# Kernel optimization log

Hardware: AMD Instinct MI355X
Metric: run time of the kernel (lower is better)

Reference implementation:

```python
import jax, jax.numpy as jnp
import numpy as np

N, E = 50000, 800000
DN, DE, H = 128, 64, 96


def _glorot(key, shape):
    fan_in = shape[0] if len(shape) > 1 else shape[0]
    return jax.random.normal(key, shape, jnp.float32) * (1.0 / np.sqrt(fan_in))


def setup_inputs() -> dict:
    key = jax.random.key(0)
    ks = jax.random.split(key, 24)
    inp = {
        "x": jax.random.normal(ks[0], (N, DN), jnp.float32),
        "edge_index": jax.random.randint(ks[1], (2, E), 0, N, jnp.int32),
        "edge_attr": jax.random.normal(ks[2], (E, DE), jnp.float32),
        # GATConv layer 0 (heads=1): lin [DN,H], lin_edge [DE,H], att vectors [H], bias [H]
        "w0": _glorot(ks[3], (DN, H)),
        "we0": _glorot(ks[4], (DE, H)),
        "as0": _glorot(ks[5], (H,)),
        "ad0": _glorot(ks[6], (H,)),
        "ae0": _glorot(ks[7], (H,)),
        "b0": jnp.zeros((H,), jnp.float32),
        # edge update 0: Linear(2H+DE -> H)
        "ew0": _glorot(ks[8], (2 * H + DE, H)),
        "eb0": jnp.zeros((H,), jnp.float32),
        # GATConv layer 1: lin [H,H], lin_edge [H,H]
        "w1": _glorot(ks[9], (H, H)),
        "we1": _glorot(ks[10], (H, H)),
        "as1": _glorot(ks[11], (H,)),
        "ad1": _glorot(ks[12], (H,)),
        "ae1": _glorot(ks[13], (H,)),
        "b1": jnp.zeros((H,), jnp.float32),
        # edge update 1: Linear(3H -> H)
        "ew1": _glorot(ks[14], (3 * H, H)),
        "eb1": jnp.zeros((H,), jnp.float32),
    }
    return inp


def gat_conv(x, src, dst, ea, W, We, a_s, a_d, a_e, b, n):
    """PyG GATConv, heads=1, eval mode, add_self_loops with fill_value='mean'."""
    ne = ea.shape[0]
    # self-loop edge attr = mean of incoming edge features per destination node
    cnt = jax.ops.segment_sum(jnp.ones((ne,), ea.dtype), dst, num_segments=n)
    loop_ea = jax.ops.segment_sum(ea, dst, num_segments=n) / jnp.maximum(cnt, 1.0)[:, None]
    ar = jnp.arange(n, dtype=src.dtype)
    sa = jnp.concatenate([src, ar])            # [E+N] augmented source idx
    da = jnp.concatenate([dst, ar])            # [E+N] augmented dest idx
    eaa = jnp.concatenate([ea, loop_ea], axis=0)
    h = x @ W                                   # [N,H]
    ep = eaa @ We                               # [E+N,H]
    logits = jax.nn.leaky_relu((h @ a_s)[sa] + (h @ a_d)[da] + ep @ a_e, 0.2)
    m = jax.ops.segment_max(logits, da, num_segments=n)
    p = jnp.exp(logits - m[da])
    denom = jax.ops.segment_sum(p, da, num_segments=n)
    alpha = p / denom[da]                       # segment softmax over dst neighborhoods
    return jax.ops.segment_sum(alpha[:, None] * h[sa], da, num_segments=n) + b


def reference(x, edge_index, edge_attr,
              w0, we0, as0, ad0, ae0, b0, ew0, eb0,
              w1, we1, as1, ad1, ae1, b1, ew1, eb1):
    src, dst = edge_index[0], edge_index[1]
    n = x.shape[0]
    # layer 0
    x = gat_conv(x, src, dst, edge_attr, w0, we0, as0, ad0, ae0, b0, n)
    edge_attr = jnp.concatenate([x[src], x[dst], edge_attr], axis=1) @ ew0 + eb0
    # layer 1
    x = gat_conv(x, src, dst, edge_attr, w1, we1, as1, ad1, ae1, b1, n)
    edge_attr = jnp.concatenate([x[src], x[dst], edge_attr], axis=1) @ ew1 + eb1
    return (x, edge_attr)
```

## Files before the change

kernel.cpp:

```cpp
#include <hip/hip_runtime.h>
#include <math.h>

#define NN 50000
#define NE 800000
#define DNODE 128
#define DEDGE 64
#define HD 96

__device__ __forceinline__ float lrelu(float x){ return x > 0.f ? x : 0.2f*x; }

__global__ void k_count(const int* __restrict__ dst, int* __restrict__ cnt){
  int e = blockIdx.x*256 + threadIdx.x;
  if (e < NE) atomicAdd(&cnt[dst[e]], 1);
}

__global__ __launch_bounds__(1024) void k_scan(const int* __restrict__ cnt,
                                               int* __restrict__ rowptr){
  __shared__ int wsum[16];
  __shared__ int carry_s;
  const int t = threadIdx.x;
  const int lane = t & 63, w = t >> 6;
  if (t == 0) carry_s = 0;
  __syncthreads();
  const int nch = (NN + 1023)/1024;
  for (int c=0;c<nch;c++){
    int i = c*1024 + t;
    int v = (i < NN) ? cnt[i] : 0;
    int s = v;
    #pragma unroll
    for (int o=1;o<64;o<<=1){
      int u = __shfl_up(s, o, 64);
      if (lane >= o) s += u;
    }
    if (lane == 63) wsum[w] = s;
    __syncthreads();
    if (t < 16){
      int x = wsum[t];
      #pragma unroll
      for (int o=1;o<16;o<<=1){
        int u = __shfl_up(x, o, 64);
        if (t >= o) x += u;
      }
      wsum[t] = x;
    }
    __syncthreads();
    int total = wsum[15];
    int base = carry_s + (w ? wsum[w-1] : 0);
    if (i < NN) rowptr[i] = base + s - v;
    __syncthreads();
    if (t == 0) carry_s += total;
  }
  __syncthreads();
  if (t == 0) rowptr[NN] = carry_s;
}

__global__ void k_fill(const int* __restrict__ src, const int* __restrict__ dst,
                       const int* __restrict__ rowptr, int* __restrict__ fillc,
                       int* __restrict__ perm, int* __restrict__ src_s){
  int e = blockIdx.x*256 + threadIdx.x;
  if (e >= NE) return;
  int d = dst[e];
  int pos = rowptr[d] + atomicAdd(&fillc[d], 1);
  perm[pos]  = e;
  src_s[pos] = src[e];
}

__global__ void k_vec(const float* __restrict__ We, const float* __restrict__ ae,
                      float* __restrict__ v, int K){
  int k = threadIdx.x;
  if (k < K){
    float s = 0.f;
    for (int j=0;j<HD;j++) s += We[k*HD + j]*ae[j];
    v[k] = s;
  }
}

__global__ void k_elr(const float* __restrict__ Ein, const float* __restrict__ v,
                      float* __restrict__ elr, int K){
  int e = blockIdx.x*256 + threadIdx.x;
  if (e >= NE) return;
  const float4* row = (const float4*)(Ein + (size_t)e*K);
  float s = 0.f;
  for (int k=0;k<K/4;k++){
    float4 a = row[k];
    float4 b = ((const float4*)v)[k];
    s += a.x*b.x + a.y*b.y + a.z*b.z + a.w*b.w;
  }
  elr[e] = s;
}

template<int K, bool DOTS>
__global__ __launch_bounds__(256,4) void k_nodegemm_t(const float* __restrict__ X,
    const float* __restrict__ W, float* __restrict__ Y, int M,
    const float* __restrict__ va, const float* __restrict__ vb,
    float* __restrict__ hs, float* __restrict__ hd){
  __shared__ float Wl[K*HD];
  for (int idx=threadIdx.x; idx<K*HD/4; idx+=256)
    ((float4*)Wl)[idx] = ((const float4*)W)[idx];
  __syncthreads();
  const int r  = threadIdx.x >> 3;
  const int c0 = (threadIdx.x & 7)*12;
  const int r0 = blockIdx.x*128 + r;
  float acc[4][12];
  #pragma unroll
  for (int q=0;q<4;q++)
    #pragma unroll
    for (int j=0;j<12;j++) acc[q][j]=0.f;
  for (int k=0;k<K;k+=4){
    float4 xv[4];
    #pragma unroll
    for (int q=0;q<4;q++){
      int row = r0 + 32*q;
      xv[q] = (row < M) ? *(const float4*)(X + (size_t)row*K + k)
                        : make_float4(0.f,0.f,0.f,0.f);
    }
    #pragma unroll
    for (int kk=0;kk<4;kk++){
      float wv[12];
      const float* wr = Wl + (k+kk)*HD + c0;
      #pragma unroll
      for (int j=0;j<12;j++) wv[j] = wr[j];
      #pragma unroll
      for (int q=0;q<4;q++){
        float xs = ((const float*)&xv[q])[kk];
        #pragma unroll
        for (int j=0;j<12;j++) acc[q][j] += xs*wv[j];
      }
    }
  }
  float vva[12], vvb[12];
  if constexpr (DOTS){
    #pragma unroll
    for (int j=0;j<12;j++){ vva[j]=va[c0+j]; vvb[j]=vb[c0+j]; }
  }
  #pragma unroll
  for (int q=0;q<4;q++){
    int row = r0 + 32*q;
    if (row >= M) continue;
    float* yr = Y + (size_t)row*HD + c0;
    float d1=0.f, d2=0.f;
    #pragma unroll
    for (int j=0;j<12;j++){
      float o = acc[q][j];
      yr[j] = o;
      if constexpr (DOTS){ d1 += o*vva[j]; d2 += o*vvb[j]; }
    }
    if constexpr (DOTS){
      #pragma unroll
      for (int o=1;o<8;o<<=1){ d1 += __shfl_xor(d1,o,64); d2 += __shfl_xor(d2,o,64); }
      if ((threadIdx.x&7)==0){ hs[row]=d1; hd[row]=d2; }
    }
  }
}

template<int K, bool ELR>
__global__ __launch_bounds__(256,4) void k_edgegemm_t(const float* __restrict__ Ein,
    const float* __restrict__ W,
    const float* __restrict__ A, const float* __restrict__ B,
    const int* __restrict__ src, const int* __restrict__ dst,
    const float* __restrict__ bias, float* __restrict__ Out,
    const float* __restrict__ v, float* __restrict__ elr){
  __shared__ float Wl[K*HD];
  for (int idx=threadIdx.x; idx<K*HD/4; idx+=256)
    ((float4*)Wl)[idx] = ((const float4*)W)[idx];
  __syncthreads();
  const int r  = threadIdx.x >> 3;
  const int c0 = (threadIdx.x & 7)*12;
  const int e0 = blockIdx.x*128 + r;
  float acc[4][12];
  #pragma unroll
  for (int q=0;q<4;q++)
    #pragma unroll
    for (int j=0;j<12;j++) acc[q][j]=0.f;
  const float* e_base = Ein + (size_t)e0*K;
  for (int k=0;k<K;k+=4){
    float4 xv[4];
    #pragma unroll
    for (int q=0;q<4;q++)
      xv[q] = *(const float4*)(e_base + (size_t)(32*q)*K + k);
    #pragma unroll
    for (int kk=0;kk<4;kk++){
      float wv[12];
      const float* wr = Wl + (k+kk)*HD + c0;
      #pragma unroll
      for (int j=0;j<12;j++) wv[j] = wr[j];
      #pragma unroll
      for (int q=0;q<4;q++){
        float xs = ((const float*)&xv[q])[kk];
        #pragma unroll
        for (int j=0;j<12;j++) acc[q][j] += xs*wv[j];
      }
    }
  }
  __syncthreads();
  float bj[12], vv[12];
  #pragma unroll
  for (int j=0;j<12;j++) bj[j] = bias[c0+j];
  if constexpr (ELR){
    #pragma unroll
    for (int j=0;j<12;j++) vv[j] = v[c0+j];
  }
  #pragma unroll
  for (int q=0;q<4;q++){
    int e = e0 + 32*q;
    int s = src[e], d = dst[e];
    const float* Ar = A + (size_t)s*HD + c0;
    const float* Br = B + (size_t)d*HD + c0;
    float* orow = Out + (size_t)e*HD + c0;
    float pd = 0.f;
    #pragma unroll
    for (int j=0;j<12;j++){
      float o = acc[q][j] + Ar[j] + Br[j] + bj[j];
      orow[j] = o;
      if constexpr (ELR) pd += o*vv[j];
    }
    if constexpr (ELR){
      pd += __shfl_xor(pd,1,64);
      pd += __shfl_xor(pd,2,64);
      pd += __shfl_xor(pd,4,64);
      if ((threadIdx.x&7)==0) elr[e] = pd;
    }
  }
}

__global__ __launch_bounds__(256) void k_gat(const int* __restrict__ rowptr,
    const int* __restrict__ src_s, const int* __restrict__ perm,
    const float* __restrict__ hs, const float* __restrict__ hd,
    const float* __restrict__ elr,
    const float* __restrict__ h, const float* __restrict__ bias,
    float* __restrict__ Out){
  int lane = threadIdx.x & 63;
  int n = blockIdx.x*4 + (threadIdx.x >> 6);
  if (n >= NN) return;
  int beg = rowptr[n], end = rowptr[n+1];
  float hdn = hd[n];
  float mxn = -INFINITY;
  float se  = 0.f;
  for (int i = beg + lane; i < end; i += 64){
    float el = elr[perm[i]];
    se += el;
    mxn = fmaxf(mxn, lrelu(hs[src_s[i]] + hdn + el));
  }
  #pragma unroll
  for (int o=32;o>0;o>>=1){
    mxn = fmaxf(mxn, __shfl_xor(mxn, o, 64));
    se += __shfl_xor(se, o, 64);
  }
  float slp = se / fmaxf((float)(end-beg), 1.f);
  float selfL = lrelu(hs[n] + hdn + slp);
  float mx = fmaxf(mxn, selfL);
  float acc0 = 0.f, acc1 = 0.f, denom = 0.f;
  for (int i = beg; i < end; ++i){
    int s = src_s[i];
    float p = __expf(lrelu(hs[s] + hdn + elr[perm[i]]) - mx);
    denom += p;
    acc0 += p * h[(size_t)s*HD + lane];
    if (lane < 32) acc1 += p * h[(size_t)s*HD + 64 + lane];
  }
  float ps = __expf(selfL - mx);
  denom += ps;
  acc0 += ps * h[(size_t)n*HD + lane];
  if (lane < 32) acc1 += ps * h[(size_t)n*HD + 64 + lane];
  float inv = 1.f/denom;
  Out[(size_t)n*HD + lane] = acc0*inv + bias[lane];
  if (lane < 32) Out[(size_t)n*HD + 64 + lane] = acc1*inv + bias[64+lane];
}

extern "C" void kernel_launch(void* const* d_in, const int* in_sizes, int n_in,
                              void* d_out, int out_size, void* d_ws, size_t ws_size,
                              hipStream_t stream){
  const float* x   = (const float*)d_in[0];
  const int*   ei  = (const int*)d_in[1];
  const float* ea  = (const float*)d_in[2];
  const float* w0  = (const float*)d_in[3];
  const float* we0 = (const float*)d_in[4];
  const float* as0 = (const float*)d_in[5];
  const float* ad0 = (const float*)d_in[6];
  const float* ae0 = (const float*)d_in[7];
  const float* b0  = (const float*)d_in[8];
  const float* ew0 = (const float*)d_in[9];
  const float* eb0 = (const float*)d_in[10];
  const float* w1  = (const float*)d_in[11];
  const float* we1 = (const float*)d_in[12];
  const float* as1 = (const float*)d_in[13];
  const float* ad1 = (const float*)d_in[14];
  const float* ae1 = (const float*)d_in[15];
  const float* b1  = (const float*)d_in[16];
  const float* ew1 = (const float*)d_in[17];
  const float* eb1 = (const float*)d_in[18];

  const int* srcp = ei;
  const int* dstp = ei + NE;

  char* ws = (char*)d_ws;
  size_t off = 0;
  auto carve = [&](size_t bytes)->char*{
    char* p = ws + off; off += (bytes + 255) & ~(size_t)255; return p;
  };
  int*   rowptr = (int*)carve(4ull*(NN+1));
  int*   fillc  = (int*)carve(4ull*NN);
  int*   perm   = (int*)carve(4ull*NE);
  int*   src_s  = (int*)carve(4ull*NE);
  float* hbuf   = (float*)carve(4ull*NN*HD);
  float* x0     = (float*)carve(4ull*NN*HD);
  float* Ab     = (float*)carve(4ull*NN*HD);
  float* Bb     = (float*)carve(4ull*NN*HD);
  float* hsb    = (float*)carve(4ull*NN);
  float* hdb    = (float*)carve(4ull*NN);
  float* elr    = (float*)carve(4ull*NE);
  float* vsm0   = (float*)carve(4ull*128);
  float* vsm1   = (float*)carve(4ull*128);
  (void)ws_size; (void)in_sizes; (void)n_in; (void)out_size;

  float* xout  = (float*)d_out;
  float* eaout = (float*)d_out + (size_t)NN*HD;

  const int EB  = (NE + 255)/256;
  const int GE  = NE/128;
  const int GN  = (NN + 127)/128;

  hipMemsetAsync(fillc, 0, 4ull*NN, stream);
  k_count<<<EB, 256, 0, stream>>>(dstp, fillc);
  k_scan<<<1, 1024, 0, stream>>>(fillc, rowptr);
  hipMemsetAsync(fillc, 0, 4ull*NN, stream);
  k_fill<<<EB, 256, 0, stream>>>(srcp, dstp, rowptr, fillc, perm, src_s);

  k_vec<<<1, 128, 0, stream>>>(we0, ae0, vsm0, DEDGE);
  k_vec<<<1, 128, 0, stream>>>(we1, ae1, vsm1, HD);

  k_elr<<<EB, 256, 0, stream>>>(ea, vsm0, elr, DEDGE);
  k_nodegemm_t<DNODE,true><<<GN, 256, 0, stream>>>(x, w0, hbuf, NN, as0, ad0, hsb, hdb);
  k_gat<<<(NN+3)/4, 256, 0, stream>>>(rowptr, src_s, perm, hsb, hdb, elr, hbuf, b0, x0);

  k_nodegemm_t<HD,false><<<GN, 256, 0, stream>>>(x0, ew0,         Ab, NN, nullptr, nullptr, nullptr, nullptr);
  k_nodegemm_t<HD,false><<<GN, 256, 0, stream>>>(x0, ew0 + 96*HD, Bb, NN, nullptr, nullptr, nullptr, nullptr);
  k_edgegemm_t<DEDGE,true><<<GE, 256, 0, stream>>>(ea, ew0 + 192*HD, Ab, Bb, srcp, dstp,
                                                   eb0, eaout, vsm1, elr);

  k_nodegemm_t<HD,true><<<GN, 256, 0, stream>>>(x0, w1, hbuf, NN, as1, ad1, hsb, hdb);
  k_gat<<<(NN+3)/4, 256, 0, stream>>>(rowptr, src_s, perm, hsb, hdb, elr, hbuf, b1, xout);

  k_nodegemm_t<HD,false><<<GN, 256, 0, stream>>>(xout, ew1,         Ab, NN, nullptr, nullptr, nullptr, nullptr);
  k_nodegemm_t<HD,false><<<GN, 256, 0, stream>>>(xout, ew1 + 96*HD, Bb, NN, nullptr, nullptr, nullptr, nullptr);
  k_edgegemm_t<HD,false><<<GE, 256, 0, stream>>>(eaout, ew1 + 192*HD, Ab, Bb, srcp, dstp,
                                                 eb1, eaout, nullptr, nullptr);
}
```

Baseline: 1.733 ms.

## Prefetch GEMM inputs and cache per-edge logits in registers for GAT aggregation

```diff
diff --git a/kernel.cpp b/kernel.cpp
--- a/kernel.cpp
+++ b/kernel.cpp
@@ -101,23 +101,31 @@
   const int r  = threadIdx.x >> 3;
   const int c0 = (threadIdx.x & 7)*12;
   const int r0 = blockIdx.x*128 + r;
+  const float* xr[4];
+  #pragma unroll
+  for (int q=0;q<4;q++){
+    int row = r0 + 32*q;
+    int rc  = row < M ? row : M-1;
+    xr[q] = X + (size_t)rc*K;
+  }
+  float vva[12], vvb[12];
+  if constexpr (DOTS){
+    #pragma unroll
+    for (int j=0;j<12;j++){ vva[j]=va[c0+j]; vvb[j]=vb[c0+j]; }
+  }
   float acc[4][12];
   #pragma unroll
   for (int q=0;q<4;q++)
     #pragma unroll
     for (int j=0;j<12;j++) acc[q][j]=0.f;
-  for (int k=0;k<K;k+=4){
-    float4 xv[4];
-    #pragma unroll
-    for (int q=0;q<4;q++){
-      int row = r0 + 32*q;
-      xv[q] = (row < M) ? *(const float4*)(X + (size_t)row*K + k)
-                        : make_float4(0.f,0.f,0.f,0.f);
-    }
+  float4 cur[4];
+  #pragma unroll
+  for (int q=0;q<4;q++) cur[q] = *(const float4*)(xr[q]);
+  auto FMAB = [&](const float4* xv, int kb){
     #pragma unroll
     for (int kk=0;kk<4;kk++){
       float wv[12];
-      const float* wr = Wl + (k+kk)*HD + c0;
+      const float* wr = Wl + (kb+kk)*HD + c0;
       #pragma unroll
       for (int j=0;j<12;j++) wv[j] = wr[j];
       #pragma unroll
@@ -127,12 +135,16 @@
         for (int j=0;j<12;j++) acc[q][j] += xs*wv[j];
       }
     }
-  }
-  float vva[12], vvb[12];
-  if constexpr (DOTS){
-    #pragma unroll
-    for (int j=0;j<12;j++){ vva[j]=va[c0+j]; vvb[j]=vb[c0+j]; }
-  }
+  };
+  for (int k=0;k<K-4;k+=4){
+    float4 nxt[4];
+    #pragma unroll
+    for (int q=0;q<4;q++) nxt[q] = *(const float4*)(xr[q] + k + 4);
+    FMAB(cur, k);
+    #pragma unroll
+    for (int q=0;q<4;q++) cur[q] = nxt[q];
+  }
+  FMAB(cur, K-4);
   #pragma unroll
   for (int q=0;q<4;q++){
     int row = r0 + 32*q;
@@ -167,21 +179,32 @@
   const int r  = threadIdx.x >> 3;
   const int c0 = (threadIdx.x & 7)*12;
   const int e0 = blockIdx.x*128 + r;
+  int sv[4], dv[4];
+  #pragma unroll
+  for (int q=0;q<4;q++){ sv[q] = src[e0+32*q]; dv[q] = dst[e0+32*q]; }
+  float bj[12], vv[12];
+  #pragma unroll
+  for (int j=0;j<12;j++) bj[j] = bias[c0+j];
+  if constexpr (ELR){
+    #pragma unroll
+    for (int j=0;j<12;j++) vv[j] = v[c0+j];
+  }
+  const float* xr[4];
+  #pragma unroll
+  for (int q=0;q<4;q++) xr[q] = Ein + (size_t)(e0 + 32*q)*K;
   float acc[4][12];
   #pragma unroll
   for (int q=0;q<4;q++)
     #pragma unroll
     for (int j=0;j<12;j++) acc[q][j]=0.f;
-  const float* e_base = Ein + (size_t)e0*K;
-  for (int k=0;k<K;k+=4){
-    float4 xv[4];
-    #pragma unroll
-    for (int q=0;q<4;q++)
-      xv[q] = *(const float4*)(e_base + (size_t)(32*q)*K + k);
+  float4 cur[4];
+  #pragma unroll
+  for (int q=0;q<4;q++) cur[q] = *(const float4*)(xr[q]);
+  auto FMAB = [&](const float4* xv, int kb){
     #pragma unroll
     for (int kk=0;kk<4;kk++){
       float wv[12];
-      const float* wr = Wl + (k+kk)*HD + c0;
+      const float* wr = Wl + (kb+kk)*HD + c0;
       #pragma unroll
       for (int j=0;j<12;j++) wv[j] = wr[j];
       #pragma unroll
@@ -191,21 +214,22 @@
         for (int j=0;j<12;j++) acc[q][j] += xs*wv[j];
       }
     }
-  }
+  };
+  for (int k=0;k<K-4;k+=4){
+    float4 nxt[4];
+    #pragma unroll
+    for (int q=0;q<4;q++) nxt[q] = *(const float4*)(xr[q] + k + 4);
+    FMAB(cur, k);
+    #pragma unroll
+    for (int q=0;q<4;q++) cur[q] = nxt[q];
+  }
+  FMAB(cur, K-4);
   __syncthreads();
-  float bj[12], vv[12];
-  #pragma unroll
-  for (int j=0;j<12;j++) bj[j] = bias[c0+j];
-  if constexpr (ELR){
-    #pragma unroll
-    for (int j=0;j<12;j++) vv[j] = v[c0+j];
-  }
   #pragma unroll
   for (int q=0;q<4;q++){
     int e = e0 + 32*q;
-    int s = src[e], d = dst[e];
-    const float* Ar = A + (size_t)s*HD + c0;
-    const float* Br = B + (size_t)d*HD + c0;
+    const float* Ar = A + (size_t)sv[q]*HD + c0;
+    const float* Br = B + (size_t)dv[q]*HD + c0;
     float* orow = Out + (size_t)e*HD + c0;
     float pd = 0.f;
     #pragma unroll
@@ -233,30 +257,64 @@
   int n = blockIdx.x*4 + (threadIdx.x >> 6);
   if (n >= NN) return;
   int beg = rowptr[n], end = rowptr[n+1];
+  int deg = end - beg;
   float hdn = hd[n];
-  float mxn = -INFINITY;
-  float se  = 0.f;
-  for (int i = beg + lane; i < end; i += 64){
-    float el = elr[perm[i]];
-    se += el;
-    mxn = fmaxf(mxn, lrelu(hs[src_s[i]] + hdn + el));
+  float mxn = -INFINITY, se = 0.f;
+  int   s_l = n;
+  float lg_l = -INFINITY;
+  for (int i0 = beg; i0 < end; i0 += 64){
+    int i = i0 + lane;
+    if (i < end){
+      int s = src_s[i];
+      float el = elr[perm[i]];
+      float lg = lrelu(hs[s] + hdn + el);
+      se += el;
+      mxn = fmaxf(mxn, lg);
+      s_l = s; lg_l = lg;
+    }
   }
   #pragma unroll
   for (int o=32;o>0;o>>=1){
     mxn = fmaxf(mxn, __shfl_xor(mxn, o, 64));
     se += __shfl_xor(se, o, 64);
   }
-  float slp = se / fmaxf((float)(end-beg), 1.f);
+  float slp = se / fmaxf((float)deg, 1.f);
   float selfL = lrelu(hs[n] + hdn + slp);
   float mx = fmaxf(mxn, selfL);
-  float acc0 = 0.f, acc1 = 0.f, denom = 0.f;
-  for (int i = beg; i < end; ++i){
-    int s = src_s[i];
-    float p = __expf(lrelu(hs[s] + hdn + elr[perm[i]]) - mx);
-    denom += p;
-    acc0 += p * h[(size_t)s*HD + lane];
-    if (lane < 32) acc1 += p * h[(size_t)s*HD + 64 + lane];
-  }
+
+  float acc0 = 0.f, acc1 = 0.f, dpart = 0.f;
+  if (deg <= 64){
+    float p_l = (lane < deg) ? __expf(lg_l - mx) : 0.f;
+    dpart = p_l;
+    #pragma unroll 4
+    for (int j=0;j<deg;j++){
+      float p = __shfl(p_l, j, 64);
+      int s   = __shfl(s_l, j, 64);
+      acc0 += p * h[(size_t)s*HD + lane];
+      if (lane < 32) acc1 += p * h[(size_t)s*HD + 64 + lane];
+    }
+  } else {
+    for (int b = beg; b < end; b += 64){
+      int cnt = min(64, end - b);
+      int sb = n; float pb = 0.f;
+      if (lane < cnt){
+        int i = b + lane;
+        sb = src_s[i];
+        pb = __expf(lrelu(hs[sb] + hdn + elr[perm[i]]) - mx);
+      }
+      dpart += pb;
+      #pragma unroll 4
+      for (int j=0;j<cnt;j++){
+        float p = __shfl(pb, j, 64);
+        int s   = __shfl(sb, j, 64);
+        acc0 += p * h[(size_t)s*HD + lane];
+        if (lane < 32) acc1 += p * h[(size_t)s*HD + 64 + lane];
+      }
+    }
+  }
+  float denom = dpart;
+  #pragma unroll
+  for (int o=32;o>0;o>>=1) denom += __shfl_xor(denom, o, 64);
   float ps = __expf(selfL - mx);
   denom += ps;
   acc0 += ps * h[(size_t)n*HD + lane];
```

Result: slower. 1.953 ms (+12.7%).
